# Kernel tuning notes

Measured on AMD Instinct MI355X. Metric: run time of the kernel, lower is better.

The kernel has to match this reference:

```python
import jax, jax.numpy as jnp
import numpy as np

N_NODES = 50000
N_EDGES = 800000
IN_DIM = 128
HID = 128
HEADS = 4
OUT_DIM = 32
NEG_SLOPE = 0.2  # DGL GATConv default


def _gat_params(key, in_dim, out_feat, heads):
    k1, k2, k3 = jax.random.split(key, 3)
    s = 1.0 / np.sqrt(in_dim)
    W = jax.random.normal(k1, (in_dim, heads * out_feat), jnp.float32) * s
    attn_l = jax.random.normal(k2, (heads, out_feat), jnp.float32) * 0.1
    attn_r = jax.random.normal(k3, (heads, out_feat), jnp.float32) * 0.1
    b = jnp.zeros((heads * out_feat,), jnp.float32)
    return W, attn_l, attn_r, b


def setup_inputs() -> dict:
    key = jax.random.key(0)
    ks = jax.random.split(key, 10)
    inp = {
        "x_am": jax.random.normal(ks[0], (N_NODES, IN_DIM), jnp.float32),
        "x_ph": jax.random.normal(ks[1], (N_NODES, IN_DIM), jnp.float32),
        "exist": jax.random.uniform(ks[2], (N_EDGES,), jnp.float32),
        "am_exist": jax.random.uniform(ks[3], (N_EDGES,), jnp.float32),
        "src": jax.random.randint(ks[4], (N_EDGES,), 0, N_NODES, jnp.int32),
        "dst": jax.random.randint(ks[5], (N_EDGES,), 0, N_NODES, jnp.int32),
    }
    # layer 0 (input_dim -> hidden//head per head), layer 1 (hidden -> output_dim per head)
    inp["W0a"], inp["al0a"], inp["ar0a"], inp["b0a"] = _gat_params(ks[6], IN_DIM, HID // HEADS, HEADS)
    inp["W0p"], inp["al0p"], inp["ar0p"], inp["b0p"] = _gat_params(ks[7], IN_DIM, HID // HEADS, HEADS)
    inp["W1a"], inp["al1a"], inp["ar1a"], inp["b1a"] = _gat_params(ks[8], HID, OUT_DIM, HEADS)
    inp["W1p"], inp["al1p"], inp["ar1p"], inp["b1p"] = _gat_params(ks[9], HID, OUT_DIM, HEADS)
    return inp


def gat_conv(x, src, dst, W, attn_l, attn_r, b, edge_w, n_nodes):
    """DGL-style GATConv with edge_weight: out[i] = sum_{e: dst=i} softmax_i(LeakyReLU(el[src]+er[dst])) * w_e * ft[src]."""
    heads, outf = attn_l.shape
    ft = (x @ W).reshape(-1, heads, outf)                 # (N, H, F)
    el = jnp.sum(ft * attn_l, axis=-1)                    # (N, H)
    er = jnp.sum(ft * attn_r, axis=-1)                    # (N, H)
    e = jax.nn.leaky_relu(el[src] + er[dst], NEG_SLOPE)   # (E, H)
    emax = jax.ops.segment_max(e, dst, num_segments=n_nodes)
    emax = jnp.where(jnp.isfinite(emax), emax, 0.0)       # guard isolated nodes
    ex = jnp.exp(e - emax[dst])
    denom = jax.ops.segment_sum(ex, dst, num_segments=n_nodes)
    a = ex / jnp.maximum(denom[dst], 1e-9)                # edge softmax over incoming edges
    a = a * edge_w[:, None]                               # post-softmax edge weighting
    out = jax.ops.segment_sum(ft[src] * a[:, :, None], dst, num_segments=n_nodes)  # (N, H, F)
    return out + b.reshape(heads, outf)


def reference(x_am, x_ph, exist, am_exist,
              W0a, al0a, ar0a, b0a, W0p, al0p, ar0p, b0p,
              W1a, al1a, ar1a, b1a, W1p, al1p, ar1p, b1p,
              src, dst):
    n = x_am.shape[0]
    # layer 0: GATConv -> flatten -> ReLU (dropout rate 0 in eval)
    h_am = gat_conv(x_am, src, dst, W0a, al0a, ar0a, b0a, am_exist, n)
    h_ph = gat_conv(x_ph, src, dst, W0p, al0p, ar0p, b0p, exist, n)
    h_am = jax.nn.relu(h_am.reshape(n, -1))
    h_ph = jax.nn.relu(h_ph.reshape(n, -1))
    # layer 1 (last): GATConv -> mean over heads
    h_am = gat_conv(h_am, src, dst, W1a, al1a, ar1a, b1a, am_exist, n).mean(axis=1)
    h_ph = gat_conv(h_ph, src, dst, W1p, al1p, ar1p, b1p, exist, n).mean(axis=1)
    return (h_am, h_ph)
```

## Files before the change

kernel.cpp:

```cpp
#include <hip/hip_runtime.h>
#include <hip/hip_fp16.h>


typedef _Float16 f16x8 __attribute__((ext_vector_type(8)));
typedef float f32x4 __attribute__((ext_vector_type(4)));

struct GemmP { const void* X; const __half* Wt; const float *al, *ar; __half* Y; float *el, *er; };
struct ChP   { const __half* ft; const float *el, *er, *bias; void* out; };

__global__ void hist_wprep_kernel(const int* __restrict__ dst, int* __restrict__ counts,
                                  int* __restrict__ rank, int E,
                                  const float* __restrict__ W0a, const float* __restrict__ W0p,
                                  const float* __restrict__ W1a, const float* __restrict__ W1p,
                                  __half* __restrict__ Wt) {
  int e = blockIdx.x * blockDim.x + threadIdx.x;
  if (e < E) rank[e] = atomicAdd(&counts[dst[e]], 1);
  if (e < 65536) {
    int m = e >> 14, i = e & 16383;
    const float* W = (m == 0) ? W0a : (m == 1) ? W0p : (m == 2) ? W1a : W1p;
    int nn = i >> 7, k = i & 127;
    Wt[(size_t)m * 16384 + nn * 128 + k] = __float2half_rn(W[k * 128 + nn]);
  }
}

__global__ __launch_bounds__(256) void scan_kernel(const int* __restrict__ counts,
                                                   int* __restrict__ offsets,
                                                   int* __restrict__ sync,
                                                   int nb_stride, int n, int E) {
  __shared__ int lds[256];
  __shared__ int sbid, sprev;
  int* state = sync + 64;
  int* agg = state + nb_stride;
  int* incl = agg + nb_stride;
  int t = threadIdx.x;
  if (t == 0) sbid = atomicAdd(sync, 1);
  __syncthreads();
  int bid = sbid;
  int i = bid * 256 + t;
  int v = (i < n) ? counts[i] : 0;
  lds[t] = v;
  __syncthreads();
  for (int off = 1; off < 256; off <<= 1) {
    int x = (t >= off) ? lds[t - off] : 0;
    __syncthreads();
    lds[t] += x;
    __syncthreads();
  }
  int total = lds[255];
  if (t == 0) {
    if (bid == 0) {
      __hip_atomic_store(&incl[0], total, __ATOMIC_RELAXED, __HIP_MEMORY_SCOPE_AGENT);
      __hip_atomic_store(&state[0], 2, __ATOMIC_RELEASE, __HIP_MEMORY_SCOPE_AGENT);
      sprev = 0;
    } else {
      __hip_atomic_store(&agg[bid], total, __ATOMIC_RELAXED, __HIP_MEMORY_SCOPE_AGENT);
      __hip_atomic_store(&state[bid], 1, __ATOMIC_RELEASE, __HIP_MEMORY_SCOPE_AGENT);
    }
  }
  if (bid > 0 && t < 64) {
    int run = 0;
    int base = bid - 1;
    while (true) {
      int idx = base - t;
      int st = 2, val = 0;
      if (idx >= 0) {
        do {
          st = __hip_atomic_load(&state[idx], __ATOMIC_ACQUIRE, __HIP_MEMORY_SCOPE_AGENT);
        } while (st == 0);
        val = (st == 2)
                  ? __hip_atomic_load(&incl[idx], __ATOMIC_RELAXED, __HIP_MEMORY_SCOPE_AGENT)
                  : __hip_atomic_load(&agg[idx], __ATOMIC_RELAXED, __HIP_MEMORY_SCOPE_AGENT);
      }
      unsigned long long done = __ballot(st == 2);
      int firstDone = (int)__ffsll(done) - 1;
      int contrib = (firstDone < 0) ? val : ((t <= firstDone) ? val : 0);
#pragma unroll
      for (int o = 1; o < 64; o <<= 1) contrib += __shfl_xor(contrib, o);
      run += contrib;
      if (firstDone >= 0) break;
      base -= 64;
    }
    if (t == 0) {
      __hip_atomic_store(&incl[bid], run + total, __ATOMIC_RELAXED, __HIP_MEMORY_SCOPE_AGENT);
      __hip_atomic_store(&state[bid], 2, __ATOMIC_RELEASE, __HIP_MEMORY_SCOPE_AGENT);
      sprev = run;
    }
  }
  __syncthreads();
  int prev = sprev;
  if (i < n) offsets[i] = prev + lds[t] - v;
  if (i == 0) offsets[n] = E;
}

__device__ __forceinline__ void fill_edges(int b0, int nfb,
                                           const int* __restrict__ src,
                                           const int* __restrict__ dst,
                                           const float* __restrict__ exist,
                                           const float* __restrict__ am_exist,
                                           const int* __restrict__ offs,
                                           const int* __restrict__ rank,
                                           int4* __restrict__ edge16, int E) {
  for (int e = b0 * 256 + threadIdx.x; e < E; e += nfb * 256) {
    int d = dst[e];
    int pos = offs[d] + rank[e];
    edge16[pos] = make_int4(src[e], d, __float_as_int(am_exist[e]), __float_as_int(exist[e]));
  }
}

__global__ void fill_kernel(const int* __restrict__ src, const int* __restrict__ dst,
                            const float* __restrict__ exist, const float* __restrict__ am_exist,
                            const int* __restrict__ offs, const int* __restrict__ rank,
                            int4* __restrict__ edge16, int E) {
  fill_edges(blockIdx.x, gridDim.x, src, dst, exist, am_exist, offs, rank, edge16, E);
}

template <int AFP16>
__device__ __forceinline__ void gemm_body(GemmP p, int bx, int n) {
  constexpr int LDH = 72;
  constexpr int LDE = 136;
  __shared__ __half lds[2 * 128 * LDH];
  __half* As = lds;
  __half* Ws = lds + 128 * LDH;
  int t = threadIdx.x;
  int row0 = bx << 7;
  int wv = t >> 6, lane = t & 63;
  int m = lane & 15, q = lane >> 4;

  f32x4 acc[2][8];
#pragma unroll
  for (int rt = 0; rt < 2; ++rt)
#pragma unroll
    for (int ct = 0; ct < 8; ++ct) acc[rt][ct] = (f32x4){0.f, 0.f, 0.f, 0.f};

#pragma unroll
  for (int kh = 0; kh < 2; ++kh) {
    __syncthreads();
    if (AFP16) {
      const __half* Xh = (const __half*)p.X;
#pragma unroll
      for (int i = 0; i < 4; ++i) {
        int c = t + (i << 8);
        int r = c >> 3, o8 = c & 7;
        uint4 v = make_uint4(0, 0, 0, 0);
        if (row0 + r < n)
          v = *(const uint4*)(Xh + (size_t)(row0 + r) * 128 + (kh << 6) + (o8 << 3));
        *(uint4*)(As + r * LDH + (o8 << 3)) = v;
      }
    } else {
      const float* Xf = (const float*)p.X;
#pragma unroll
      for (int i = 0; i < 8; ++i) {
        int c = t + (i << 8);
        int r = c >> 4, f4 = c & 15;
        float4 v = make_float4(0.f, 0.f, 0.f, 0.f);
        if (row0 + r < n)
          v = *(const float4*)(Xf + (size_t)(row0 + r) * 128 + (kh << 6) + (f4 << 2));
        union { __half h[4]; uint2 u; } pk;
        pk.h[0] = __float2half_rn(v.x); pk.h[1] = __float2half_rn(v.y);
        pk.h[2] = __float2half_rn(v.z); pk.h[3] = __float2half_rn(v.w);
        *(uint2*)(As + r * LDH + (f4 << 2)) = pk.u;
      }
    }
#pragma unroll
    for (int i = 0; i < 4; ++i) {
      int c = t + (i << 8);
      int r = c >> 3, o8 = c & 7;
      uint4 v = *(const uint4*)(p.Wt + (size_t)r * 128 + (kh << 6) + (o8 << 3));
      *(uint4*)(Ws + r * LDH + (o8 << 3)) = v;
    }
    __syncthreads();
#pragma unroll
    for (int kc = 0; kc < 2; ++kc) {
      f16x8 a0 = *(const f16x8*)(As + (wv * 32 + m) * LDH + kc * 32 + q * 8);
      f16x8 a1 = *(const f16x8*)(As + (wv * 32 + 16 + m) * LDH + kc * 32 + q * 8);
#pragma unroll
      for (int ct = 0; ct < 8; ++ct) {
        f16x8 b = *(const f16x8*)(Ws + (ct * 16 + m) * LDH + kc * 32 + q * 8);
        acc[0][ct] = __builtin_amdgcn_mfma_f32_16x16x32_f16(a0, b, acc[0][ct], 0, 0, 0);
        acc[1][ct] = __builtin_amdgcn_mfma_f32_16x16x32_f16(a1, b, acc[1][ct], 0, 0, 0);
      }
    }
  }
  __syncthreads();
#pragma unroll
  for (int rt = 0; rt < 2; ++rt) {
    int rbase = wv * 32 + rt * 16 + q * 4;
#pragma unroll
    for (int ct = 0; ct < 8; ++ct) {
      int col = ct * 16 + m;
#pragma unroll
      for (int r = 0; r < 4; ++r)
        lds[(rbase + r) * LDE + col] = __float2half_rn(acc[rt][ct][r]);
    }
  }
  __syncthreads();
  {
    int r = t & 127;
    int half = t >> 7;
    int row = row0 + r;
    if (row < n) {
      float e0 = 0.f, e1 = 0.f, r0 = 0.f, r1 = 0.f;
#pragma unroll
      for (int i = 0; i < 8; ++i) {
        int cbase = half * 64 + i * 8;
        f16x8 v = *(const f16x8*)(lds + r * LDE + cbase);
        *(uint4*)(p.Y + (size_t)row * 128 + cbase) = *(const uint4*)&v;
#pragma unroll
        for (int j = 0; j < 8; ++j) {
          float f = (float)v[j];
          float av = p.al[cbase + j];
          float rv = p.ar[cbase + j];
          if (((i * 8 + j) >> 5) == 0) { e0 = fmaf(f, av, e0); r0 = fmaf(f, rv, r0); }
          else                         { e1 = fmaf(f, av, e1); r1 = fmaf(f, rv, r1); }
        }
      }
      *(float2*)(p.el + (size_t)row * 4 + half * 2) = make_float2(e0, e1);
      *(float2*)(p.er + (size_t)row * 4 + half * 2) = make_float2(r0, r1);
    }
  }
}

template <int AFP16>
__global__ __launch_bounds__(256) void gemm_kernel(GemmP p0, GemmP p1, int n) {
  gemm_body<AFP16>(blockIdx.y ? p1 : p0, blockIdx.x, n);
}

__global__ __launch_bounds__(256) void fill_gemm0_kernel(
    GemmP p0, GemmP p1, int gg, int n, int nfb,
    const int* __restrict__ src, const int* __restrict__ dst,
    const float* __restrict__ exist, const float* __restrict__ am_exist,
    const int* __restrict__ offs, const int* __restrict__ rank,
    int4* __restrict__ edge16, int E) {
  int b = blockIdx.x;
  if (b < nfb) {
    fill_edges(b, nfb, src, dst, exist, am_exist, offs, rank, edge16, E);
    return;
  }
  int g = b - nfb;
  gemm_body<0>((g >= gg) ? p1 : p0, (g >= gg) ? g - gg : g, n);
}

template <int LAYER>
__global__ __launch_bounds__(256) void gather_kernel(ChP c0, ChP c1,
                                                     const int* __restrict__ offs,
                                                     const int4* __restrict__ edge16, int n) {
  int t = threadIdx.x;
  int w = t >> 6;
  int lane = t & 63;
  int node = blockIdx.x * 2 + (w >> 1);
  int ch = w & 1;
  if (node >= n) return;
  ChP P = ch ? c1 : c0;
  int hh = lane >> 4;
  int ce = lane & 7;

  int start = __builtin_amdgcn_readfirstlane(offs[node]);
  int end = __builtin_amdgcn_readfirstlane(offs[node + 1]);
  float er_h = P.er[(size_t)node * 4 + hh];
  const __half2* ftbase = (const __half2*)P.ft;
  const float* elb = P.el;
  const int* e32 = (const int*)edge16;

  float acc0 = 0.f, acc1 = 0.f, l = 0.f;
  int k = start;
  while (k + 8 <= end) {
    int4 ed[8];
#pragma unroll
    for (int j = 0; j < 8; ++j) ed[j] = edge16[k + j];
    int s_v = e32[(size_t)(k + ce) * 4];
    float el_v = elb[(size_t)s_v * 4 + hh];
    float ev = el_v + er_h;
    ev = (ev > 0.f) ? ev : 0.2f * ev;
    float x_v = __expf(ev);
#pragma unroll
    for (int j = 0; j < 8; ++j) {
      int s = ed[j].x;
      float wgt = __int_as_float(ch ? ed[j].w : ed[j].z);
      __half2 fh = ftbase[(size_t)s * 64 + lane];
      float x = __shfl(x_v, j, 16);
      l += x;
      float cv = x * wgt;
      acc0 = fmaf(cv, __low2float(fh), acc0);
      acc1 = fmaf(cv, __high2float(fh), acc1);
    }
    k += 8;
  }
  for (; k < end; ++k) {
    int4 ed = edge16[k];
    int s = ed.x;
    float wgt = __int_as_float(ch ? ed.w : ed.z);
    float el_s = elb[(size_t)s * 4 + hh];
    float ev = el_s + er_h;
    ev = (ev > 0.f) ? ev : 0.2f * ev;
    float x = __expf(ev);
    __half2 fh = ftbase[(size_t)s * 64 + lane];
    l += x;
    float cv = x * wgt;
    acc0 = fmaf(cv, __low2float(fh), acc0);
    acc1 = fmaf(cv, __high2float(fh), acc1);
  }

  float rl = 1.f / fmaxf(l, 1e-9f);
  float2 b2 = *(const float2*)(P.bias + lane * 2);
  float v0 = fmaf(acc0, rl, b2.x);
  float v1 = fmaf(acc1, rl, b2.y);
  if (LAYER == 0) {
    __half2 h = __floats2half2_rn(fmaxf(v0, 0.f), fmaxf(v1, 0.f));
    ((__half2*)P.out)[(size_t)node * 64 + lane] = h;
  } else {
    v0 += __shfl_xor(v0, 16); v1 += __shfl_xor(v1, 16);
    v0 += __shfl_xor(v0, 32); v1 += __shfl_xor(v1, 32);
    if (lane < 16) {
      *(float2*)((float*)P.out + (size_t)node * 32 + lane * 2) =
          make_float2(0.25f * v0, 0.25f * v1);
    }
  }
}

extern "C" void kernel_launch(void* const* d_in, const int* in_sizes, int n_in,
                              void* d_out, int out_size, void* d_ws, size_t ws_size,
                              hipStream_t stream) {
  const float* x_am = (const float*)d_in[0];
  const float* x_ph = (const float*)d_in[1];
  const float* exist = (const float*)d_in[2];
  const float* am_exist = (const float*)d_in[3];
  const int* src = (const int*)d_in[4];
  const int* dst = (const int*)d_in[5];
  const float* W0a = (const float*)d_in[6];
  const float* al0a = (const float*)d_in[7];
  const float* ar0a = (const float*)d_in[8];
  const float* b0a = (const float*)d_in[9];
  const float* W0p = (const float*)d_in[10];
  const float* al0p = (const float*)d_in[11];
  const float* ar0p = (const float*)d_in[12];
  const float* b0p = (const float*)d_in[13];
  const float* W1a = (const float*)d_in[14];
  const float* al1a = (const float*)d_in[15];
  const float* ar1a = (const float*)d_in[16];
  const float* b1a = (const float*)d_in[17];
  const float* W1p = (const float*)d_in[18];
  const float* al1p = (const float*)d_in[19];
  const float* ar1p = (const float*)d_in[20];
  const float* b1p = (const float*)d_in[21];

  int n = in_sizes[0] / 128;
  int E = in_sizes[2];
  int N_pad = (n + 255) & ~255;
  int nb = (n + 255) / 256;
  int NB_pad = (nb + 63) & ~63;

  size_t szN = (size_t)N_pad * 4;
  size_t szSync = (size_t)(64 + 3 * NB_pad) * 4;
  size_t szRank = (size_t)E * 4;
  size_t szOffs = (size_t)(N_pad + 8) * 4;
  size_t szE16 = (size_t)E * 16;
  size_t szFt16 = (size_t)n * 128 * 2;
  size_t szEl = (size_t)N_pad * 4 * 4;
  size_t szWt = (size_t)4 * 128 * 128 * 2;

  auto rnd = [](size_t b) { return (b + 255) & ~(size_t)255; };
  size_t fixed = rnd(szN) + rnd(szSync) + rnd(szRank) + rnd(szOffs) + rnd(szE16) +
                 4 * rnd(szEl) + rnd(szWt);
  bool dual = ws_size >= fixed + 4 * rnd(szFt16);

  char* p = (char*)d_ws;
  auto take = [&](size_t b) { char* q = p; p += (b + 255) & ~(size_t)255; return q; };
  int* counts = (int*)take(szN);
  int* sync = (int*)take(szSync);
  int* rank = (int*)take(szRank);
  int* offs = (int*)take(szOffs);
  int4* edge16 = (int4*)take(szE16);
  __half* Wt = (__half*)take(szWt);
  float* el_am = (float*)take(szEl);
  float* el_ph = (float*)take(szEl);
  float* er_am = (float*)take(szEl);
  float* er_ph = (float*)take(szEl);
  __half* ft_am = (__half*)take(szFt16);
  __half* ft_ph = dual ? (__half*)take(szFt16) : ft_am;
  __half* hb_am = (__half*)take(szFt16);
  __half* hb_ph = dual ? (__half*)take(szFt16) : hb_am;

  float* out_am = (float*)d_out;
  float* out_ph = out_am + (size_t)n * 32;

  (void)hipMemsetAsync(counts, 0, rnd(szN) + rnd(szSync), stream);
  hist_wprep_kernel<<<(E + 255) / 256, 256, 0, stream>>>(dst, counts, rank, E,
                                                         W0a, W0p, W1a, W1p, Wt);
  scan_kernel<<<nb, 256, 0, stream>>>(counts, offs, sync, NB_pad, n, E);

  int gg = (n + 127) / 128;
  int gw = (n + 1) / 2;
  GemmP g0a{x_am, Wt,          al0a, ar0a, ft_am, el_am, er_am};
  GemmP g0p{x_ph, Wt + 16384,  al0p, ar0p, ft_ph, el_ph, er_ph};
  GemmP g1a{hb_am, Wt + 32768, al1a, ar1a, ft_am, el_am, er_am};
  GemmP g1p{hb_ph, Wt + 49152, al1p, ar1p, ft_ph, el_ph, er_ph};
  ChP c0a{ft_am, el_am, er_am, b0a, hb_am};
  ChP c0p{ft_ph, el_ph, er_ph, b0p, hb_ph};
  ChP c1a{ft_am, el_am, er_am, b1a, out_am};
  ChP c1p{ft_ph, el_ph, er_ph, b1p, out_ph};

  if (dual) {
    constexpr int NFB = 256;
    fill_gemm0_kernel<<<NFB + 2 * gg, 256, 0, stream>>>(
        g0a, g0p, gg, n, NFB, src, dst, exist, am_exist, offs, rank, edge16, E);
    gather_kernel<0><<<gw, 256, 0, stream>>>(c0a, c0p, offs, edge16, n);
    gemm_kernel<1><<<dim3(gg, 2), 256, 0, stream>>>(g1a, g1p, n);
    gather_kernel<1><<<gw, 256, 0, stream>>>(c1a, c1p, offs, edge16, n);
  } else {
    fill_kernel<<<(E + 255) / 256, 256, 0, stream>>>(src, dst, exist, am_exist,
                                                     offs, rank, edge16, E);
    gemm_kernel<0><<<dim3(gg, 2), 256, 0, stream>>>(g0a, g0a, n);
    gather_kernel<0><<<gw, 256, 0, stream>>>(c0a, c0a, offs, edge16, n);
    gemm_kernel<1><<<dim3(gg, 2), 256, 0, stream>>>(g1a, g1a, n);
    gather_kernel<1><<<gw, 256, 0, stream>>>(c1a, c1a, offs, edge16, n);
    gemm_kernel<0><<<dim3(gg, 2), 256, 0, stream>>>(g0p, g0p, n);
    gather_kernel<0><<<gw, 256, 0, stream>>>(c0p, c0p, offs, edge16, n);
    gemm_kernel<1><<<dim3(gg, 2), 256, 0, stream>>>(g1p, g1p, n);
    gather_kernel<1><<<gw, 256, 0, stream>>>(c1p, c1p, offs, edge16, n);
  }
}
```

Measured before the change: 402.9 us.

## Split CSR edge records per channel and overlap histogram with layer-0 GEMM

Replaces the 16-byte edge record (src,dst,w_am,w_ph) with two 8-byte per-channel arrays (src,weight), so each gather wave reads half the edge bytes. The dst histogram now runs in the same launch as the layer-0 GEMM, and a small init kernel replaces the memset and does the weight transpose. The fill step becomes a separate launch after the scan instead of overlapping the GEMM. The fill kernel writes twice as many records, and the launch count and ordering change.

```diff
diff --git a/kernel.cpp b/kernel.cpp
--- a/kernel.cpp
+++ b/kernel.cpp
@@ -6,19 +6,18 @@
 typedef float f32x4 __attribute__((ext_vector_type(4)));
 
 struct GemmP { const void* X; const __half* Wt; const float *al, *ar; __half* Y; float *el, *er; };
-struct ChP   { const __half* ft; const float *el, *er, *bias; void* out; };
-
-__global__ void hist_wprep_kernel(const int* __restrict__ dst, int* __restrict__ counts,
-                                  int* __restrict__ rank, int E,
-                                  const float* __restrict__ W0a, const float* __restrict__ W0p,
-                                  const float* __restrict__ W1a, const float* __restrict__ W1p,
-                                  __half* __restrict__ Wt) {
-  int e = blockIdx.x * blockDim.x + threadIdx.x;
-  if (e < E) rank[e] = atomicAdd(&counts[dst[e]], 1);
-  if (e < 65536) {
-    int m = e >> 14, i = e & 16383;
+struct ChP   { const __half* ft; const float *el, *er, *bias; const int2* ed; void* out; };
+
+__global__ void init_kernel(int* __restrict__ zero, int nzero,
+                            const float* __restrict__ W0a, const float* __restrict__ W0p,
+                            const float* __restrict__ W1a, const float* __restrict__ W1p,
+                            __half* __restrict__ Wt) {
+  int i = blockIdx.x * 256 + threadIdx.x;
+  if (i < nzero) zero[i] = 0;
+  {
+    int m = i >> 14, idx = i & 16383;
     const float* W = (m == 0) ? W0a : (m == 1) ? W0p : (m == 2) ? W1a : W1p;
-    int nn = i >> 7, k = i & 127;
+    int nn = idx >> 7, k = idx & 127;
     Wt[(size_t)m * 16384 + nn * 128 + k] = __float2half_rn(W[k * 128 + nn]);
   }
 }
@@ -92,26 +91,17 @@
   if (i == 0) offsets[n] = E;
 }
 
-__device__ __forceinline__ void fill_edges(int b0, int nfb,
-                                           const int* __restrict__ src,
-                                           const int* __restrict__ dst,
-                                           const float* __restrict__ exist,
-                                           const float* __restrict__ am_exist,
-                                           const int* __restrict__ offs,
-                                           const int* __restrict__ rank,
-                                           int4* __restrict__ edge16, int E) {
-  for (int e = b0 * 256 + threadIdx.x; e < E; e += nfb * 256) {
-    int d = dst[e];
-    int pos = offs[d] + rank[e];
-    edge16[pos] = make_int4(src[e], d, __float_as_int(am_exist[e]), __float_as_int(exist[e]));
-  }
-}
-
 __global__ void fill_kernel(const int* __restrict__ src, const int* __restrict__ dst,
                             const float* __restrict__ exist, const float* __restrict__ am_exist,
                             const int* __restrict__ offs, const int* __restrict__ rank,
-                            int4* __restrict__ edge16, int E) {
-  fill_edges(blockIdx.x, gridDim.x, src, dst, exist, am_exist, offs, rank, edge16, E);
+                            int2* __restrict__ am8, int2* __restrict__ ph8, int E) {
+  int e = blockIdx.x * blockDim.x + threadIdx.x;
+  if (e >= E) return;
+  int d = dst[e];
+  int pos = offs[d] + rank[e];
+  int s = src[e];
+  am8[pos] = make_int2(s, __float_as_int(am_exist[e]));
+  ph8[pos] = make_int2(s, __float_as_int(exist[e]));
 }
 
 template <int AFP16>
@@ -225,25 +215,22 @@
   gemm_body<AFP16>(blockIdx.y ? p1 : p0, blockIdx.x, n);
 }
 
-__global__ __launch_bounds__(256) void fill_gemm0_kernel(
-    GemmP p0, GemmP p1, int gg, int n, int nfb,
-    const int* __restrict__ src, const int* __restrict__ dst,
-    const float* __restrict__ exist, const float* __restrict__ am_exist,
-    const int* __restrict__ offs, const int* __restrict__ rank,
-    int4* __restrict__ edge16, int E) {
+__global__ __launch_bounds__(256) void hist_gemm0_kernel(
+    GemmP p0, GemmP p1, int gg, int n,
+    const int* __restrict__ dst, int* __restrict__ counts,
+    int* __restrict__ rank, int E) {
   int b = blockIdx.x;
-  if (b < nfb) {
-    fill_edges(b, nfb, src, dst, exist, am_exist, offs, rank, edge16, E);
+  if (b < 2 * gg) {
+    gemm_body<0>((b >= gg) ? p1 : p0, (b >= gg) ? b - gg : b, n);
     return;
   }
-  int g = b - nfb;
-  gemm_body<0>((g >= gg) ? p1 : p0, (g >= gg) ? g - gg : g, n);
+  int e = (b - 2 * gg) * 256 + threadIdx.x;
+  if (e < E) rank[e] = atomicAdd(&counts[dst[e]], 1);
 }
 
 template <int LAYER>
 __global__ __launch_bounds__(256) void gather_kernel(ChP c0, ChP c1,
-                                                     const int* __restrict__ offs,
-                                                     const int4* __restrict__ edge16, int n) {
+                                                     const int* __restrict__ offs, int n) {
   int t = threadIdx.x;
   int w = t >> 6;
   int lane = t & 63;
@@ -259,15 +246,16 @@
   float er_h = P.er[(size_t)node * 4 + hh];
   const __half2* ftbase = (const __half2*)P.ft;
   const float* elb = P.el;
-  const int* e32 = (const int*)edge16;
+  const int2* edb = P.ed;
+  const int* e32 = (const int*)edb;
 
   float acc0 = 0.f, acc1 = 0.f, l = 0.f;
   int k = start;
   while (k + 8 <= end) {
-    int4 ed[8];
-#pragma unroll
-    for (int j = 0; j < 8; ++j) ed[j] = edge16[k + j];
-    int s_v = e32[(size_t)(k + ce) * 4];
+    int2 ed[8];
+#pragma unroll
+    for (int j = 0; j < 8; ++j) ed[j] = edb[k + j];
+    int s_v = e32[(size_t)(k + ce) * 2];
     float el_v = elb[(size_t)s_v * 4 + hh];
     float ev = el_v + er_h;
     ev = (ev > 0.f) ? ev : 0.2f * ev;
@@ -275,7 +263,7 @@
 #pragma unroll
     for (int j = 0; j < 8; ++j) {
       int s = ed[j].x;
-      float wgt = __int_as_float(ch ? ed[j].w : ed[j].z);
+      float wgt = __int_as_float(ed[j].y);
       __half2 fh = ftbase[(size_t)s * 64 + lane];
       float x = __shfl(x_v, j, 16);
       l += x;
@@ -286,9 +274,9 @@
     k += 8;
   }
   for (; k < end; ++k) {
-    int4 ed = edge16[k];
+    int2 ed = edb[k];
     int s = ed.x;
-    float wgt = __int_as_float(ch ? ed.w : ed.z);
+    float wgt = __int_as_float(ed.y);
     float el_s = elb[(size_t)s * 4 + hh];
     float ev = el_s + er_h;
     ev = (ev > 0.f) ? ev : 0.2f * ev;
@@ -353,13 +341,13 @@
   size_t szSync = (size_t)(64 + 3 * NB_pad) * 4;
   size_t szRank = (size_t)E * 4;
   size_t szOffs = (size_t)(N_pad + 8) * 4;
-  size_t szE16 = (size_t)E * 16;
+  size_t szE8 = (size_t)E * 8;
   size_t szFt16 = (size_t)n * 128 * 2;
   size_t szEl = (size_t)N_pad * 4 * 4;
   size_t szWt = (size_t)4 * 128 * 128 * 2;
 
   auto rnd = [](size_t b) { return (b + 255) & ~(size_t)255; };
-  size_t fixed = rnd(szN) + rnd(szSync) + rnd(szRank) + rnd(szOffs) + rnd(szE16) +
+  size_t fixed = rnd(szN) + rnd(szSync) + rnd(szRank) + rnd(szOffs) + 2 * rnd(szE8) +
                  4 * rnd(szEl) + rnd(szWt);
   bool dual = ws_size >= fixed + 4 * rnd(szFt16);
 
@@ -369,7 +357,8 @@
   int* sync = (int*)take(szSync);
   int* rank = (int*)take(szRank);
   int* offs = (int*)take(szOffs);
-  int4* edge16 = (int4*)take(szE16);
+  int2* am8 = (int2*)take(szE8);
+  int2* ph8 = (int2*)take(szE8);
   __half* Wt = (__half*)take(szWt);
   float* el_am = (float*)take(szEl);
   float* el_ph = (float*)take(szEl);
@@ -383,39 +372,42 @@
   float* out_am = (float*)d_out;
   float* out_ph = out_am + (size_t)n * 32;
 
-  (void)hipMemsetAsync(counts, 0, rnd(szN) + rnd(szSync), stream);
-  hist_wprep_kernel<<<(E + 255) / 256, 256, 0, stream>>>(dst, counts, rank, E,
-                                                         W0a, W0p, W1a, W1p, Wt);
-  scan_kernel<<<nb, 256, 0, stream>>>(counts, offs, sync, NB_pad, n, E);
-
+  int nzero = (int)((rnd(szN) + rnd(szSync)) / 4);
   int gg = (n + 127) / 128;
   int gw = (n + 1) / 2;
+  int nhb = (E + 255) / 256;
   GemmP g0a{x_am, Wt,          al0a, ar0a, ft_am, el_am, er_am};
   GemmP g0p{x_ph, Wt + 16384,  al0p, ar0p, ft_ph, el_ph, er_ph};
   GemmP g1a{hb_am, Wt + 32768, al1a, ar1a, ft_am, el_am, er_am};
   GemmP g1p{hb_ph, Wt + 49152, al1p, ar1p, ft_ph, el_ph, er_ph};
-  ChP c0a{ft_am, el_am, er_am, b0a, hb_am};
-  ChP c0p{ft_ph, el_ph, er_ph, b0p, hb_ph};
-  ChP c1a{ft_am, el_am, er_am, b1a, out_am};
-  ChP c1p{ft_ph, el_ph, er_ph, b1p, out_ph};
+  ChP c0a{ft_am, el_am, er_am, b0a, am8, hb_am};
+  ChP c0p{ft_ph, el_ph, er_ph, b0p, ph8, hb_ph};
+  ChP c1a{ft_am, el_am, er_am, b1a, am8, out_am};
+  ChP c1p{ft_ph, el_ph, er_ph, b1p, ph8, out_ph};
+
+  init_kernel<<<256, 256, 0, stream>>>(counts, nzero, W0a, W0p, W1a, W1p, Wt);
 
   if (dual) {
-    constexpr int NFB = 256;
-    fill_gemm0_kernel<<<NFB + 2 * gg, 256, 0, stream>>>(
-        g0a, g0p, gg, n, NFB, src, dst, exist, am_exist, offs, rank, edge16, E);
-    gather_kernel<0><<<gw, 256, 0, stream>>>(c0a, c0p, offs, edge16, n);
+    hist_gemm0_kernel<<<2 * gg + nhb, 256, 0, stream>>>(g0a, g0p, gg, n,
+                                                        dst, counts, rank, E);
+    scan_kernel<<<nb, 256, 0, stream>>>(counts, offs, sync, NB_pad, n, E);
+    fill_kernel<<<nhb, 256, 0, stream>>>(src, dst, exist, am_exist, offs, rank,
+                                         am8, ph8, E);
+    gather_kernel<0><<<gw, 256, 0, stream>>>(c0a, c0p, offs, n);
     gemm_kernel<1><<<dim3(gg, 2), 256, 0, stream>>>(g1a, g1p, n);
-    gather_kernel<1><<<gw, 256, 0, stream>>>(c1a, c1p, offs, edge16, n);
+    gather_kernel<1><<<gw, 256, 0, stream>>>(c1a, c1p, offs, n);
   } else {
-    fill_kernel<<<(E + 255) / 256, 256, 0, stream>>>(src, dst, exist, am_exist,
-                                                     offs, rank, edge16, E);
-    gemm_kernel<0><<<dim3(gg, 2), 256, 0, stream>>>(g0a, g0a, n);
-    gather_kernel<0><<<gw, 256, 0, stream>>>(c0a, c0a, offs, edge16, n);
+    hist_gemm0_kernel<<<2 * gg + nhb, 256, 0, stream>>>(g0a, g0a, gg, n,
+                                                        dst, counts, rank, E);
+    scan_kernel<<<nb, 256, 0, stream>>>(counts, offs, sync, NB_pad, n, E);
+    fill_kernel<<<nhb, 256, 0, stream>>>(src, dst, exist, am_exist, offs, rank,
+                                         am8, ph8, E);
+    gather_kernel<0><<<gw, 256, 0, stream>>>(c0a, c0a, offs, n);
     gemm_kernel<1><<<dim3(gg, 2), 256, 0, stream>>>(g1a, g1a, n);
-    gather_kernel<1><<<gw, 256, 0, stream>>>(c1a, c1a, offs, edge16, n);
+    gather_kernel<1><<<gw, 256, 0, stream>>>(c1a, c1a, offs, n);
     gemm_kernel<0><<<dim3(gg, 2), 256, 0, stream>>>(g0p, g0p, n);
-    gather_kernel<0><<<gw, 256, 0, stream>>>(c0p, c0p, offs, edge16, n);
+    gather_kernel<0><<<gw, 256, 0, stream>>>(c0p, c0p, offs, n);
     gemm_kernel<1><<<dim3(gg, 2), 256, 0, stream>>>(g1p, g1p, n);
-    gather_kernel<1><<<gw, 256, 0, stream>>>(c1p, c1p, offs, edge16, n);
-  }
-}
+    gather_kernel<1><<<gw, 256, 0, stream>>>(c1p, c1p, offs, n);
+  }
+}
```

After: 423.8 us. 5.2% more time.
